# Optimization experiments

Measured on AMD Instinct MI355X. Metric: run time of the kernel, lower is better.

## Reference

```python
import jax, jax.numpy as jnp
import numpy as np

B, T, D = 2, 2048, 1024
N, H = 16, 64  # num_heads, head_dim
LOG2E = 1.442695041
NEG_INF = -1.0e9


def setup_inputs() -> dict:
    key = jax.random.key(0)
    ks = jax.random.split(key, 6)
    return {
        "input_tensor": jax.random.normal(ks[0], (B, T, D), dtype=jnp.float32),
        "attention_mask": jax.random.randint(ks[1], (B, 1, T, T), 0, 2, dtype=jnp.int32),
        "wq": jax.random.normal(ks[2], (D, N, H), dtype=jnp.float32),
        "bq": jnp.zeros((N, H), dtype=jnp.float32),
        "wk": jax.random.normal(ks[3], (D, N, H), dtype=jnp.float32),
        "bk": jnp.zeros((N, H), dtype=jnp.float32),
        "wv": jax.random.normal(ks[4], (D, N, H), dtype=jnp.float32),
        "bv": jnp.zeros((N, H), dtype=jnp.float32),
        "wo": jax.random.normal(ks[5], (D, N, H), dtype=jnp.float32),
        "bo": jnp.zeros((D,), dtype=jnp.float32),
        "per_dim_scale": jnp.zeros((H,), dtype=jnp.float32),
    }


def reference(input_tensor, attention_mask, wq, bq, wk, bk, wv, bv, wo, bo, per_dim_scale):
    # QKV projections: [B,T,D] x [D,N,H] -> [B,T,N,H]
    q = jnp.einsum('btd,dnh->btnh', input_tensor, wq) + bq
    k = jnp.einsum('btd,dnh->btnh', input_tensor, wk) + bk
    v = jnp.einsum('btd,dnh->btnh', input_tensor, wv) + bv
    # per-dim query scaling: (log2(e)/sqrt(H)) * softplus(per_dim_scale)
    scale = (LOG2E / jnp.sqrt(jnp.asarray(H, q.dtype))) * jax.nn.softplus(per_dim_scale)
    q = q * scale
    # scores: [B,N,T,S]
    scores = jnp.einsum('btnh,bsnh->bnts', q, k)
    scores = jnp.where(attention_mask == 0, jnp.asarray(NEG_INF, scores.dtype), scores)
    weights = jax.nn.softmax(scores, axis=-1)
    # AV: [B,N,T,S] x [B,S,N,H] -> [B,T,N,H]
    attn_out = jnp.einsum('bnts,bsnh->btnh', weights, v)
    # output projection: [B,T,N,H] x [D,N,H] -> [B,T,D]
    return jnp.einsum('btnh,dnh->btd', attn_out, wo) + bo
```

## Files before the change

kernel.cpp:

```cpp
#include <hip/hip_runtime.h>
#include <math.h>

typedef __bf16 bf16;
typedef __attribute__((ext_vector_type(8))) __bf16 bf16x8;
typedef __attribute__((ext_vector_type(4))) __bf16 bf16x4;
typedef __attribute__((ext_vector_type(4))) float f32x4;

#define BB 2
#define TT 2048
#define DD 1024
#define NHD 16
#define HD 64
#define MM (BB*TT)
#define LOG2E_F 1.442695041f
#define NEGINF_F (-1.0e9f)

__device__ __forceinline__ void gld16(const bf16* g, bf16* l)
{
    __builtin_amdgcn_global_load_lds(
        (const __attribute__((address_space(1))) unsigned int*)g,
        (__attribute__((address_space(3))) unsigned int*)l, 16, 0, 0);
}

__global__ __launch_bounds__(256)
void split_x(const float* __restrict__ in, bf16* __restrict__ hi,
             bf16* __restrict__ lo, int n4)
{
    int i = blockIdx.x * 256 + threadIdx.x;
    if (i < n4) {
        float4 v = ((const float4*)in)[i];
        float f[4] = {v.x, v.y, v.z, v.w};
        bf16x4 h, l;
        #pragma unroll
        for (int j = 0; j < 4; ++j) {
            bf16 hh = (bf16)f[j];
            h[j] = hh;
            l[j] = (bf16)(f[j] - (float)hh);
        }
        *(bf16x4*)(hi + (size_t)i * 4) = h;
        *(bf16x4*)(lo + (size_t)i * 4) = l;
    }
}

__global__ __launch_bounds__(256)
void prep_weights(const float* __restrict__ wq, const float* __restrict__ wk,
                  const float* __restrict__ wv, const float* __restrict__ wo,
                  bf16* __restrict__ qkh, bf16* __restrict__ qkl,
                  bf16* __restrict__ vh, bf16* __restrict__ ob)
{
    __shared__ float tile[32][33];
    const int z  = blockIdx.z;
    const int t  = threadIdx.x;
    const int r  = t >> 3;
    const int c4 = (t & 7) << 2;
    const int bx = blockIdx.x << 5;
    const int by = blockIdx.y << 5;
    if (z == 3) {
        float4 v = *(const float4*)(wo + (size_t)(by + r) * 1024 + bx + c4);
        bf16x4 o = { (bf16)v.x, (bf16)v.y, (bf16)v.z, (bf16)v.w };
        *(bf16x4*)(ob + (size_t)(by + r) * 1024 + bx + c4) = o;
        return;
    }
    const float* src = (z == 0) ? wq : ((z == 1) ? wk : wv);
    bf16* oh = (z == 0) ? qkh : ((z == 1) ? qkh + 1048576 : vh);
    bf16* ol = (z == 0) ? qkl : ((z == 1) ? qkl + 1048576 : nullptr);

    float4 v = *(const float4*)(src + (size_t)(by + r) * 1024 + bx + c4);
    tile[r][c4+0] = v.x; tile[r][c4+1] = v.y; tile[r][c4+2] = v.z; tile[r][c4+3] = v.w;
    __syncthreads();
    bf16x4 hv, lv;
    #pragma unroll
    for (int j = 0; j < 4; ++j) {
        float f = tile[c4 + j][r];
        bf16 h = (bf16)f;
        hv[j] = h;
        lv[j] = (bf16)(f - (float)h);
    }
    *(bf16x4*)(oh + (size_t)(bx + r) * 1024 + by + c4) = hv;
    if (ol)
        *(bf16x4*)(ol + (size_t)(bx + r) * 1024 + by + c4) = lv;
}

__global__ __launch_bounds__(256)
void pack_mask(const int* __restrict__ m, unsigned* __restrict__ bits, int n)
{
    int i = blockIdx.x * 256 + threadIdx.x;
    int lane = threadIdx.x & 63;
    int v = (i < n) ? m[i] : 0;
    unsigned long long b = __ballot(v != 0);
    if ((lane & 31) == 0 && i < n)
        bits[i >> 5] = (unsigned)(b >> (lane & 32));
}

__global__ __launch_bounds__(256)
void gemm128(const bf16* __restrict__ A0, const bf16* __restrict__ A1,
             const bf16* __restrict__ A2, const bf16* __restrict__ B0,
             const bf16* __restrict__ B1, const bf16* __restrict__ B2,
             const int nseg,
             const float* __restrict__ bias1, const float* __restrict__ bias2,
             const float* __restrict__ pds,
             bf16* __restrict__ oQh, bf16* __restrict__ oQl,
             bf16* __restrict__ oKh, bf16* __restrict__ oKl,
             bf16* __restrict__ oVt, float* __restrict__ oF,
             const int mode)
{
    __shared__ bf16 As[128 * 32];
    __shared__ bf16 Bs[128 * 32];

    const int t    = threadIdx.x;
    const int lane = t & 63;
    const int w    = t >> 6;
    const int quad = lane >> 4, l15 = lane & 15;
    const int m0   = blockIdx.y << 7;
    const int n0   = blockIdx.x << 7;
    const int wm   = (w >> 1) << 6;
    const int wn   = (w & 1)  << 6;

    const int jr0 = ((w * 2 + 0) << 4) + (lane >> 2);
    const int jr1 = ((w * 2 + 1) << 4) + (lane >> 2);
    const int kch = (lane & 3) << 3;

    bf16* lA0 = As + (w * 2 + 0) * 512;
    bf16* lA1 = As + (w * 2 + 1) * 512;
    bf16* lB0 = Bs + (w * 2 + 0) * 512;
    bf16* lB1 = Bs + (w * 2 + 1) * 512;

    f32x4 acc[4][4] = {};

    const bf16* Aseg[3] = {A0, A1, A2};
    const bf16* Bseg[3] = {B0, B1, B2};

    for (int seg = 0; seg < nseg; ++seg) {
        const bf16* Ap0 = Aseg[seg] + (size_t)(m0 + jr0) * DD + kch;
        const bf16* Ap1 = Aseg[seg] + (size_t)(m0 + jr1) * DD + kch;
        const bf16* Bp0 = Bseg[seg] + (size_t)(n0 + jr0) * DD + kch;
        const bf16* Bp1 = Bseg[seg] + (size_t)(n0 + jr1) * DD + kch;
        for (int k0 = 0; k0 < DD; k0 += 32) {
            __syncthreads();
            gld16(Ap0 + k0, lA0);
            gld16(Ap1 + k0, lA1);
            gld16(Bp0 + k0, lB0);
            gld16(Bp1 + k0, lB1);
            __syncthreads();
            bf16x8 af[4], bfm[4];
            #pragma unroll
            for (int mt = 0; mt < 4; ++mt)
                af[mt] = *(const bf16x8*)(As + (wm + (mt << 4) + l15) * 32 + (quad << 3));
            #pragma unroll
            for (int nt = 0; nt < 4; ++nt)
                bfm[nt] = *(const bf16x8*)(Bs + (wn + (nt << 4) + l15) * 32 + (quad << 3));
            #pragma unroll
            for (int mt = 0; mt < 4; ++mt)
                #pragma unroll
                for (int nt = 0; nt < 4; ++nt)
                    acc[mt][nt] = __builtin_amdgcn_mfma_f32_16x16x32_bf16(
                        af[mt], bfm[nt], acc[mt][nt], 0, 0, 0);
        }
    }

    if (mode == 0) {
        #pragma unroll
        for (int nt = 0; nt < 4; ++nt) {
            const int col = n0 + wn + (nt << 4) + l15;
            const int isQ = (col < 1024);
            const int nh  = col & 1023;
            const int n   = nh >> 6, h = nh & 63;
            const float bcol = isQ ? bias1[nh] : bias2[nh];
            float s = 1.f;
            if (isQ) {
                float x  = pds[h];
                float sp = fmaxf(x, 0.f) + log1pf(expf(-fabsf(x)));
                s = (LOG2E_F * LOG2E_F / 8.0f) * sp;
            }
            bf16* dH = isQ ? oQh : oKh;
            bf16* dL = isQ ? oQl : oKl;
            #pragma unroll
            for (int mt = 0; mt < 4; ++mt) {
                #pragma unroll
                for (int reg = 0; reg < 4; ++reg) {
                    const int row = m0 + wm + (mt << 4) + (quad << 2) + reg;
                    const int bi  = row >> 11;
                    const int tt  = row & (TT - 1);
                    float val = (acc[mt][nt][reg] + bcol) * s;
                    const size_t idx = (((size_t)bi * NHD + n) * TT + tt) * HD + h;
                    bf16 hi = (bf16)val;
                    dH[idx] = hi;
                    dL[idx] = (bf16)(val - (float)hi);
                }
            }
        }
    } else if (mode == 1) {
        #pragma unroll
        for (int nt = 0; nt < 4; ++nt) {
            const int col = n0 + wn + (nt << 4) + l15;
            const int bi  = col >> 11;
            const int tt  = col & (TT - 1);
            #pragma unroll
            for (int mt = 0; mt < 4; ++mt) {
                #pragma unroll
                for (int reg = 0; reg < 4; ++reg) {
                    const int row = m0 + wm + (mt << 4) + (quad << 2) + reg;
                    float val = acc[mt][nt][reg] + bias1[row];
                    oVt[((size_t)bi * 1024 + row) * TT + tt] = (bf16)val;
                }
            }
        }
    } else {
        #pragma unroll
        for (int nt = 0; nt < 4; ++nt) {
            const int col = n0 + wn + (nt << 4) + l15;
            const float bcol = bias2[col];
            #pragma unroll
            for (int mt = 0; mt < 4; ++mt) {
                #pragma unroll
                for (int reg = 0; reg < 4; ++reg) {
                    const int row = m0 + wm + (mt << 4) + (quad << 2) + reg;
                    oF[(size_t)row * DD + col] = acc[mt][nt][reg] + bcol;
                }
            }
        }
    }
}

__global__ __launch_bounds__(256)
void attn_mfma(const bf16* __restrict__ Qh, const bf16* __restrict__ Ql,
               const bf16* __restrict__ Kh, const bf16* __restrict__ Kl,
               const bf16* __restrict__ Vt, const unsigned* __restrict__ mbits,
               bf16* __restrict__ AO)
{
    __shared__ bf16 Ksh[64][72];
    __shared__ bf16 Ksl[64][72];
    __shared__ bf16 Vts[64][72];
    __shared__ bf16 Ps[4][16][72];
    __shared__ unsigned msk[64][2];

    const int t    = threadIdx.x;
    const int lane = t & 63;
    const int w    = t >> 6;
    const int quad = lane >> 4, l15 = lane & 15;
    const int bn   = blockIdx.y;
    const int b    = bn >> 4, n = bn & 15;
    const int q0   = blockIdx.x << 6;

    const bf16* Qbh = Qh + (size_t)bn * TT * HD;
    const bf16* Qbl = Ql + (size_t)bn * TT * HD;
    const bf16* Kbh = Kh + (size_t)bn * TT * HD;
    const bf16* Kbl = Kl + (size_t)bn * TT * HD;
    const bf16* Vtb = Vt + (size_t)bn * HD * TT;

    const int qrow = q0 + (w << 4) + l15;
    bf16x8 qfh[2], qfl[2];
    qfh[0] = *(const bf16x8*)(Qbh + (size_t)qrow * HD + (quad << 3));
    qfh[1] = *(const bf16x8*)(Qbh + (size_t)qrow * HD + 32 + (quad << 3));
    qfl[0] = *(const bf16x8*)(Qbl + (size_t)qrow * HD + (quad << 3));
    qfl[1] = *(const bf16x8*)(Qbl + (size_t)qrow * HD + 32 + (quad << 3));

    f32x4 O[4];
    #pragma unroll
    for (int i = 0; i < 4; ++i) O[i] = (f32x4){0.f,0.f,0.f,0.f};
    float m_i = -INFINITY;
    float l_i = 0.f;

    const int rS = t >> 2, cS = (t & 3) << 4;

    for (int kb = 0; kb < TT; kb += 64) {
        const bf16* kph = Kbh + (size_t)(kb + rS) * HD + cS;
        const bf16* kpl = Kbl + (size_t)(kb + rS) * HD + cS;
        bf16x8 kh0 = *(const bf16x8*)kph;
        bf16x8 kh1 = *(const bf16x8*)(kph + 8);
        bf16x8 kl0 = *(const bf16x8*)kpl;
        bf16x8 kl1 = *(const bf16x8*)(kpl + 8);
        const bf16* vp = Vtb + (size_t)rS * TT + kb + cS;
        bf16x8 v0v = *(const bf16x8*)vp;
        bf16x8 v1v = *(const bf16x8*)(vp + 8);
        unsigned mw = 0;
        if (t < 128)
            mw = mbits[((size_t)b * TT + q0 + (t >> 1)) * (TT / 32) + (kb >> 5) + (t & 1)];

        __syncthreads();
        *(bf16x8*)&Ksh[rS][cS]     = kh0;
        *(bf16x8*)&Ksh[rS][cS + 8] = kh1;
        *(bf16x8*)&Ksl[rS][cS]     = kl0;
        *(bf16x8*)&Ksl[rS][cS + 8] = kl1;
        *(bf16x8*)&Vts[rS][cS]     = v0v;
        *(bf16x8*)&Vts[rS][cS + 8] = v1v;
        if (t < 128) msk[t >> 1][t & 1] = mw;
        __syncthreads();

        f32x4 s_acc[4];
        #pragma unroll
        for (int i = 0; i < 4; ++i) s_acc[i] = (f32x4){0.f,0.f,0.f,0.f};
        #pragma unroll
        for (int k2 = 0; k2 < 2; ++k2) {
            #pragma unroll
            for (int nt = 0; nt < 4; ++nt) {
                bf16x8 bkh = *(const bf16x8*)&Ksh[(nt << 4) + l15][(k2 << 5) + (quad << 3)];
                bf16x8 bkl = *(const bf16x8*)&Ksl[(nt << 4) + l15][(k2 << 5) + (quad << 3)];
                s_acc[nt] = __builtin_amdgcn_mfma_f32_16x16x32_bf16(bkh, qfh[k2], s_acc[nt], 0, 0, 0);
                s_acc[nt] = __builtin_amdgcn_mfma_f32_16x16x32_bf16(bkl, qfh[k2], s_acc[nt], 0, 0, 0);
                s_acc[nt] = __builtin_amdgcn_mfma_f32_16x16x32_bf16(bkh, qfl[k2], s_acc[nt], 0, 0, 0);
            }
        }

        const unsigned w0 = msk[(w << 4) + l15][0];
        const unsigned w1 = msk[(w << 4) + l15][1];
        float sv[16];
        #pragma unroll
        for (int nt = 0; nt < 4; ++nt) {
            const unsigned word = (nt & 2) ? w1 : w0;
            #pragma unroll
            for (int reg = 0; reg < 4; ++reg) {
                const int bit = ((nt & 1) << 4) + (quad << 2) + reg;
                sv[nt * 4 + reg] = ((word >> bit) & 1u) ? s_acc[nt][reg] : NEGINF_F;
            }
        }
        float mx = sv[0];
        #pragma unroll
        for (int i = 1; i < 16; ++i) mx = fmaxf(mx, sv[i]);
        mx = fmaxf(mx, __shfl_xor(mx, 16));
        mx = fmaxf(mx, __shfl_xor(mx, 32));
        const float mnew  = fmaxf(m_i, mx);
        const float alpha = exp2f(m_i - mnew);
        float p[16], sum = 0.f;
        #pragma unroll
        for (int i = 0; i < 16; ++i) { p[i] = exp2f(sv[i] - mnew); sum += p[i]; }
        sum += __shfl_xor(sum, 16);
        sum += __shfl_xor(sum, 32);
        l_i = l_i * alpha + sum;
        m_i = mnew;
        #pragma unroll
        for (int nt = 0; nt < 4; ++nt) {
            O[nt][0] *= alpha; O[nt][1] *= alpha;
            O[nt][2] *= alpha; O[nt][3] *= alpha;
            #pragma unroll
            for (int reg = 0; reg < 4; ++reg)
                Ps[w][l15][(nt << 4) + (quad << 2) + reg] = (bf16)p[nt * 4 + reg];
        }

        #pragma unroll
        for (int s2 = 0; s2 < 2; ++s2) {
            bf16x8 ap = *(const bf16x8*)&Ps[w][l15][(s2 << 5) + (quad << 3)];
            #pragma unroll
            for (int nt = 0; nt < 4; ++nt) {
                bf16x8 bv = *(const bf16x8*)&Vts[(nt << 4) + l15][(s2 << 5) + (quad << 3)];
                O[nt] = __builtin_amdgcn_mfma_f32_16x16x32_bf16(bv, ap, O[nt], 0, 0, 0);
            }
        }
    }

    {
        const float inv = 1.0f / l_i;
        const size_t base = ((size_t)b * TT + qrow) * (NHD * HD) + (size_t)n * HD;
        #pragma unroll
        for (int nt = 0; nt < 4; ++nt) {
            bf16x4 o = { (bf16)(O[nt][0] * inv), (bf16)(O[nt][1] * inv),
                         (bf16)(O[nt][2] * inv), (bf16)(O[nt][3] * inv) };
            *(bf16x4*)(AO + base + (nt << 4) + (quad << 2)) = o;
        }
    }
}

extern "C" void kernel_launch(void* const* d_in, const int* in_sizes, int n_in,
                              void* d_out, int out_size, void* d_ws, size_t ws_size,
                              hipStream_t stream)
{
    const float* X   = (const float*)d_in[0];
    const int*   msk = (const int*)d_in[1];
    const float* wq  = (const float*)d_in[2];
    const float* bq  = (const float*)d_in[3];
    const float* wk  = (const float*)d_in[4];
    const float* bk  = (const float*)d_in[5];
    const float* wv  = (const float*)d_in[6];
    const float* bv  = (const float*)d_in[7];
    const float* wo  = (const float*)d_in[8];
    const float* bo  = (const float*)d_in[9];
    const float* pds = (const float*)d_in[10];
    float* out = (float*)d_out;

    bf16* ws   = (bf16*)d_ws;
    bf16* Xh   = ws;
    bf16* Xl   = ws + 4194304;
    bf16* WQKh = ws + 8388608;
    bf16* WQKl = ws + 10485760;
    bf16* Wvh  = ws + 12582912;
    bf16* Wob  = ws + 13631488;
    bf16* Qhb  = ws + 14680064;
    bf16* Qlb  = ws + 18874368;
    bf16* Khb  = ws + 23068672;
    bf16* Klb  = ws + 27262976;
    unsigned* mbits = (unsigned*)(ws + 31457280);
    bf16* Vtb  = Xl;
    bf16* AOb  = Xh;

    dim3 blk(256);

    split_x<<<4096, blk, 0, stream>>>(X, Xh, Xl, MM * DD / 4);
    prep_weights<<<dim3(32, 32, 4), blk, 0, stream>>>(wq, wk, wv, wo,
                                                      WQKh, WQKl, Wvh, Wob);
    pack_mask<<<32768, blk, 0, stream>>>(msk, mbits, BB * TT * TT);

    gemm128<<<dim3(16, 32), blk, 0, stream>>>(
        Xh, Xh, Xl, WQKh, WQKl, WQKh, 3, bq, bk, pds,
        Qhb, Qlb, Khb, Klb, nullptr, nullptr, 0);

    gemm128<<<dim3(32, 8), blk, 0, stream>>>(
        Wvh, nullptr, nullptr, Xh, nullptr, nullptr, 1, bv, nullptr, nullptr,
        nullptr, nullptr, nullptr, nullptr, Vtb, nullptr, 1);

    dim3 ga(TT / 64, BB * NHD);
    attn_mfma<<<ga, blk, 0, stream>>>(Qhb, Qlb, Khb, Klb, Vtb, mbits, AOb);

    gemm128<<<dim3(8, 32), blk, 0, stream>>>(
        AOb, nullptr, nullptr, Wob, nullptr, nullptr, 1, nullptr, bo, nullptr,
        nullptr, nullptr, nullptr, nullptr, nullptr, out, 2);
}
```

Before: 366.7 us.

## Merge prep kernels into one launch and fuse split-bf16 QK GEMM segments

Replaces three preprocessing kernels (X split, weight transpose/split, mask packing) with a single launch dispatched by block index, which removes launch gaps. The QK projection gets a dedicated kernel that loads hi and lo tiles of X and W together in each k-step and issues three MFMA passes per tile. Before, the three split-precision segments ran as separate k loops. This cuts the number of barriers and k-loop iterations, at the cost of twice the LDS per block, which may lower occupancy. The attention kernel also now writes P to LDS with vectorized bf16x4 stores instead of scalar stores.

Measured after the change: 344.5 us. 1.06x faster.

```diff
diff --git a/kernel.cpp b/kernel.cpp
--- a/kernel.cpp
+++ b/kernel.cpp
@@ -23,12 +23,21 @@
 }
 
 __global__ __launch_bounds__(256)
-void split_x(const float* __restrict__ in, bf16* __restrict__ hi,
-             bf16* __restrict__ lo, int n4)
-{
-    int i = blockIdx.x * 256 + threadIdx.x;
-    if (i < n4) {
-        float4 v = ((const float4*)in)[i];
+void prep_all(const float* __restrict__ X, const int* __restrict__ m,
+              const float* __restrict__ wq, const float* __restrict__ wk,
+              const float* __restrict__ wv, const float* __restrict__ wo,
+              bf16* __restrict__ Xh, bf16* __restrict__ Xl,
+              bf16* __restrict__ qkh, bf16* __restrict__ qkl,
+              bf16* __restrict__ vh, bf16* __restrict__ ob,
+              unsigned* __restrict__ bits)
+{
+    __shared__ float tile[32][33];
+    const int bid = blockIdx.x;
+    const int t   = threadIdx.x;
+
+    if (bid < 4096) {
+        int i = bid * 256 + t;
+        float4 v = ((const float4*)X)[i];
         float f[4] = {v.x, v.y, v.z, v.w};
         bf16x4 h, l;
         #pragma unroll
@@ -37,75 +46,65 @@
             h[j] = hh;
             l[j] = (bf16)(f[j] - (float)hh);
         }
-        *(bf16x4*)(hi + (size_t)i * 4) = h;
-        *(bf16x4*)(lo + (size_t)i * 4) = l;
+        *(bf16x4*)(Xh + (size_t)i * 4) = h;
+        *(bf16x4*)(Xl + (size_t)i * 4) = l;
+        return;
+    }
+    if (bid < 8192) {
+        const int idx = bid - 4096;
+        const int z   = idx >> 10;
+        const int bx  = (idx & 31) << 5;
+        const int by  = ((idx >> 5) & 31) << 5;
+        const int r   = t >> 3;
+        const int c4  = (t & 7) << 2;
+        if (z == 3) {
+            float4 v = *(const float4*)(wo + (size_t)(by + r) * 1024 + bx + c4);
+            bf16x4 o = { (bf16)v.x, (bf16)v.y, (bf16)v.z, (bf16)v.w };
+            *(bf16x4*)(ob + (size_t)(by + r) * 1024 + bx + c4) = o;
+            return;
+        }
+        const float* src = (z == 0) ? wq : ((z == 1) ? wk : wv);
+        bf16* oh = (z == 0) ? qkh : ((z == 1) ? qkh + 1048576 : vh);
+        bf16* ol = (z == 0) ? qkl : ((z == 1) ? qkl + 1048576 : nullptr);
+        float4 v = *(const float4*)(src + (size_t)(by + r) * 1024 + bx + c4);
+        tile[r][c4+0] = v.x; tile[r][c4+1] = v.y;
+        tile[r][c4+2] = v.z; tile[r][c4+3] = v.w;
+        __syncthreads();
+        bf16x4 hv, lv;
+        #pragma unroll
+        for (int j = 0; j < 4; ++j) {
+            float f = tile[c4 + j][r];
+            bf16 h = (bf16)f;
+            hv[j] = h;
+            lv[j] = (bf16)(f - (float)h);
+        }
+        *(bf16x4*)(oh + (size_t)(bx + r) * 1024 + by + c4) = hv;
+        if (ol)
+            *(bf16x4*)(ol + (size_t)(bx + r) * 1024 + by + c4) = lv;
+        return;
+    }
+    {
+        int i = (bid - 8192) * 256 + t;
+        int lane = t & 63;
+        int v = m[i];
+        unsigned long long bl = __ballot(v != 0);
+        if ((lane & 31) == 0)
+            bits[i >> 5] = (unsigned)(bl >> (lane & 32));
     }
 }
 
 __global__ __launch_bounds__(256)
-void prep_weights(const float* __restrict__ wq, const float* __restrict__ wk,
-                  const float* __restrict__ wv, const float* __restrict__ wo,
-                  bf16* __restrict__ qkh, bf16* __restrict__ qkl,
-                  bf16* __restrict__ vh, bf16* __restrict__ ob)
-{
-    __shared__ float tile[32][33];
-    const int z  = blockIdx.z;
-    const int t  = threadIdx.x;
-    const int r  = t >> 3;
-    const int c4 = (t & 7) << 2;
-    const int bx = blockIdx.x << 5;
-    const int by = blockIdx.y << 5;
-    if (z == 3) {
-        float4 v = *(const float4*)(wo + (size_t)(by + r) * 1024 + bx + c4);
-        bf16x4 o = { (bf16)v.x, (bf16)v.y, (bf16)v.z, (bf16)v.w };
-        *(bf16x4*)(ob + (size_t)(by + r) * 1024 + bx + c4) = o;
-        return;
-    }
-    const float* src = (z == 0) ? wq : ((z == 1) ? wk : wv);
-    bf16* oh = (z == 0) ? qkh : ((z == 1) ? qkh + 1048576 : vh);
-    bf16* ol = (z == 0) ? qkl : ((z == 1) ? qkl + 1048576 : nullptr);
-
-    float4 v = *(const float4*)(src + (size_t)(by + r) * 1024 + bx + c4);
-    tile[r][c4+0] = v.x; tile[r][c4+1] = v.y; tile[r][c4+2] = v.z; tile[r][c4+3] = v.w;
-    __syncthreads();
-    bf16x4 hv, lv;
-    #pragma unroll
-    for (int j = 0; j < 4; ++j) {
-        float f = tile[c4 + j][r];
-        bf16 h = (bf16)f;
-        hv[j] = h;
-        lv[j] = (bf16)(f - (float)h);
-    }
-    *(bf16x4*)(oh + (size_t)(bx + r) * 1024 + by + c4) = hv;
-    if (ol)
-        *(bf16x4*)(ol + (size_t)(bx + r) * 1024 + by + c4) = lv;
-}
-
-__global__ __launch_bounds__(256)
-void pack_mask(const int* __restrict__ m, unsigned* __restrict__ bits, int n)
-{
-    int i = blockIdx.x * 256 + threadIdx.x;
-    int lane = threadIdx.x & 63;
-    int v = (i < n) ? m[i] : 0;
-    unsigned long long b = __ballot(v != 0);
-    if ((lane & 31) == 0 && i < n)
-        bits[i >> 5] = (unsigned)(b >> (lane & 32));
-}
-
-__global__ __launch_bounds__(256)
-void gemm128(const bf16* __restrict__ A0, const bf16* __restrict__ A1,
-             const bf16* __restrict__ A2, const bf16* __restrict__ B0,
-             const bf16* __restrict__ B1, const bf16* __restrict__ B2,
-             const int nseg,
-             const float* __restrict__ bias1, const float* __restrict__ bias2,
+void gemm_qk(const bf16* __restrict__ Xh, const bf16* __restrict__ Xl,
+             const bf16* __restrict__ Wh, const bf16* __restrict__ Wl,
+             const float* __restrict__ bq, const float* __restrict__ bk,
              const float* __restrict__ pds,
              bf16* __restrict__ oQh, bf16* __restrict__ oQl,
-             bf16* __restrict__ oKh, bf16* __restrict__ oKl,
-             bf16* __restrict__ oVt, float* __restrict__ oF,
-             const int mode)
-{
-    __shared__ bf16 As[128 * 32];
-    __shared__ bf16 Bs[128 * 32];
+             bf16* __restrict__ oKh, bf16* __restrict__ oKl)
+{
+    __shared__ bf16 Ah[128 * 32];
+    __shared__ bf16 Al[128 * 32];
+    __shared__ bf16 Bh[128 * 32];
+    __shared__ bf16 Bl[128 * 32];
 
     const int t    = threadIdx.x;
     const int lane = t & 63;
@@ -120,96 +119,175 @@
     const int jr1 = ((w * 2 + 1) << 4) + (lane >> 2);
     const int kch = (lane & 3) << 3;
 
+    bf16* lAh0 = Ah + (w * 2 + 0) * 512;  bf16* lAh1 = Ah + (w * 2 + 1) * 512;
+    bf16* lAl0 = Al + (w * 2 + 0) * 512;  bf16* lAl1 = Al + (w * 2 + 1) * 512;
+    bf16* lBh0 = Bh + (w * 2 + 0) * 512;  bf16* lBh1 = Bh + (w * 2 + 1) * 512;
+    bf16* lBl0 = Bl + (w * 2 + 0) * 512;  bf16* lBl1 = Bl + (w * 2 + 1) * 512;
+
+    const bf16* pAh0 = Xh + (size_t)(m0 + jr0) * DD + kch;
+    const bf16* pAh1 = Xh + (size_t)(m0 + jr1) * DD + kch;
+    const bf16* pAl0 = Xl + (size_t)(m0 + jr0) * DD + kch;
+    const bf16* pAl1 = Xl + (size_t)(m0 + jr1) * DD + kch;
+    const bf16* pBh0 = Wh + (size_t)(n0 + jr0) * DD + kch;
+    const bf16* pBh1 = Wh + (size_t)(n0 + jr1) * DD + kch;
+    const bf16* pBl0 = Wl + (size_t)(n0 + jr0) * DD + kch;
+    const bf16* pBl1 = Wl + (size_t)(n0 + jr1) * DD + kch;
+
+    f32x4 acc[4][4] = {};
+
+    for (int k0 = 0; k0 < DD; k0 += 32) {
+        __syncthreads();
+        gld16(pAh0 + k0, lAh0);  gld16(pAh1 + k0, lAh1);
+        gld16(pAl0 + k0, lAl0);  gld16(pAl1 + k0, lAl1);
+        gld16(pBh0 + k0, lBh0);  gld16(pBh1 + k0, lBh1);
+        gld16(pBl0 + k0, lBl0);  gld16(pBl1 + k0, lBl1);
+        __syncthreads();
+
+        bf16x8 ah[4], bh[4];
+        #pragma unroll
+        for (int mt = 0; mt < 4; ++mt)
+            ah[mt] = *(const bf16x8*)(Ah + (wm + (mt << 4) + l15) * 32 + (quad << 3));
+        #pragma unroll
+        for (int nt = 0; nt < 4; ++nt)
+            bh[nt] = *(const bf16x8*)(Bh + (wn + (nt << 4) + l15) * 32 + (quad << 3));
+        #pragma unroll
+        for (int mt = 0; mt < 4; ++mt)
+            #pragma unroll
+            for (int nt = 0; nt < 4; ++nt)
+                acc[mt][nt] = __builtin_amdgcn_mfma_f32_16x16x32_bf16(
+                    ah[mt], bh[nt], acc[mt][nt], 0, 0, 0);
+
+        bf16x8 bl[4];
+        #pragma unroll
+        for (int nt = 0; nt < 4; ++nt)
+            bl[nt] = *(const bf16x8*)(Bl + (wn + (nt << 4) + l15) * 32 + (quad << 3));
+        #pragma unroll
+        for (int mt = 0; mt < 4; ++mt)
+            #pragma unroll
+            for (int nt = 0; nt < 4; ++nt)
+                acc[mt][nt] = __builtin_amdgcn_mfma_f32_16x16x32_bf16(
+                    ah[mt], bl[nt], acc[mt][nt], 0, 0, 0);
+
+        bf16x8 al[4];
+        #pragma unroll
+        for (int mt = 0; mt < 4; ++mt)
+            al[mt] = *(const bf16x8*)(Al + (wm + (mt << 4) + l15) * 32 + (quad << 3));
+        #pragma unroll
+        for (int mt = 0; mt < 4; ++mt)
+            #pragma unroll
+            for (int nt = 0; nt < 4; ++nt)
+                acc[mt][nt] = __builtin_amdgcn_mfma_f32_16x16x32_bf16(
+                    al[mt], bh[nt], acc[mt][nt], 0, 0, 0);
+    }
+
+    #pragma unroll
+    for (int nt = 0; nt < 4; ++nt) {
+        const int col = n0 + wn + (nt << 4) + l15;
+        const int isQ = (col < 1024);
+        const int nh  = col & 1023;
+        const int n   = nh >> 6, h = nh & 63;
+        const float bcol = isQ ? bq[nh] : bk[nh];
+        float s = 1.f;
+        if (isQ) {
+            float x  = pds[h];
+            float sp = fmaxf(x, 0.f) + log1pf(expf(-fabsf(x)));
+            s = (LOG2E_F * LOG2E_F / 8.0f) * sp;
+        }
+        bf16* dH = isQ ? oQh : oKh;
+        bf16* dL = isQ ? oQl : oKl;
+        #pragma unroll
+        for (int mt = 0; mt < 4; ++mt) {
+            #pragma unroll
+            for (int reg = 0; reg < 4; ++reg) {
+                const int row = m0 + wm + (mt << 4) + (quad << 2) + reg;
+                const int bi  = row >> 11;
+                const int tt  = row & (TT - 1);
+                float val = (acc[mt][nt][reg] + bcol) * s;
+                const size_t idx = (((size_t)bi * NHD + n) * TT + tt) * HD + h;
+                bf16 hi = (bf16)val;
+                dH[idx] = hi;
+                dL[idx] = (bf16)(val - (float)hi);
+            }
+        }
+    }
+}
+
+__global__ __launch_bounds__(256)
+void gemm128(const bf16* __restrict__ A, const bf16* __restrict__ Bt,
+             const float* __restrict__ bias,
+             bf16* __restrict__ oVt, float* __restrict__ oF, const int mode)
+{
+    __shared__ bf16 As[128 * 32];
+    __shared__ bf16 Bs[128 * 32];
+
+    const int t    = threadIdx.x;
+    const int lane = t & 63;
+    const int w    = t >> 6;
+    const int quad = lane >> 4, l15 = lane & 15;
+    const int m0   = blockIdx.y << 7;
+    const int n0   = blockIdx.x << 7;
+    const int wm   = (w >> 1) << 6;
+    const int wn   = (w & 1)  << 6;
+
+    const int jr0 = ((w * 2 + 0) << 4) + (lane >> 2);
+    const int jr1 = ((w * 2 + 1) << 4) + (lane >> 2);
+    const int kch = (lane & 3) << 3;
+
     bf16* lA0 = As + (w * 2 + 0) * 512;
     bf16* lA1 = As + (w * 2 + 1) * 512;
     bf16* lB0 = Bs + (w * 2 + 0) * 512;
     bf16* lB1 = Bs + (w * 2 + 1) * 512;
 
+    const bf16* Ap0 = A  + (size_t)(m0 + jr0) * DD + kch;
+    const bf16* Ap1 = A  + (size_t)(m0 + jr1) * DD + kch;
+    const bf16* Bp0 = Bt + (size_t)(n0 + jr0) * DD + kch;
+    const bf16* Bp1 = Bt + (size_t)(n0 + jr1) * DD + kch;
+
     f32x4 acc[4][4] = {};
 
-    const bf16* Aseg[3] = {A0, A1, A2};
-    const bf16* Bseg[3] = {B0, B1, B2};
-
-    for (int seg = 0; seg < nseg; ++seg) {
-        const bf16* Ap0 = Aseg[seg] + (size_t)(m0 + jr0) * DD + kch;
-        const bf16* Ap1 = Aseg[seg] + (size_t)(m0 + jr1) * DD + kch;
-        const bf16* Bp0 = Bseg[seg] + (size_t)(n0 + jr0) * DD + kch;
-        const bf16* Bp1 = Bseg[seg] + (size_t)(n0 + jr1) * DD + kch;
-        for (int k0 = 0; k0 < DD; k0 += 32) {
-            __syncthreads();
-            gld16(Ap0 + k0, lA0);
-            gld16(Ap1 + k0, lA1);
-            gld16(Bp0 + k0, lB0);
-            gld16(Bp1 + k0, lB1);
-            __syncthreads();
-            bf16x8 af[4], bfm[4];
-            #pragma unroll
-            for (int mt = 0; mt < 4; ++mt)
-                af[mt] = *(const bf16x8*)(As + (wm + (mt << 4) + l15) * 32 + (quad << 3));
+    for (int k0 = 0; k0 < DD; k0 += 32) {
+        __syncthreads();
+        gld16(Ap0 + k0, lA0);
+        gld16(Ap1 + k0, lA1);
+        gld16(Bp0 + k0, lB0);
+        gld16(Bp1 + k0, lB1);
+        __syncthreads();
+        bf16x8 af[4], bfm[4];
+        #pragma unroll
+        for (int mt = 0; mt < 4; ++mt)
+            af[mt] = *(const bf16x8*)(As + (wm + (mt << 4) + l15) * 32 + (quad << 3));
+        #pragma unroll
+        for (int nt = 0; nt < 4; ++nt)
+            bfm[nt] = *(const bf16x8*)(Bs + (wn + (nt << 4) + l15) * 32 + (quad << 3));
+        #pragma unroll
+        for (int mt = 0; mt < 4; ++mt)
             #pragma unroll
             for (int nt = 0; nt < 4; ++nt)
-                bfm[nt] = *(const bf16x8*)(Bs + (wn + (nt << 4) + l15) * 32 + (quad << 3));
-            #pragma unroll
-            for (int mt = 0; mt < 4; ++mt)
-                #pragma unroll
-                for (int nt = 0; nt < 4; ++nt)
-                    acc[mt][nt] = __builtin_amdgcn_mfma_f32_16x16x32_bf16(
-                        af[mt], bfm[nt], acc[mt][nt], 0, 0, 0);
-        }
-    }
-
-    if (mode == 0) {
+                acc[mt][nt] = __builtin_amdgcn_mfma_f32_16x16x32_bf16(
+                    af[mt], bfm[nt], acc[mt][nt], 0, 0, 0);
+    }
+
+    if (mode == 1) {
         #pragma unroll
         for (int nt = 0; nt < 4; ++nt) {
             const int col = n0 + wn + (nt << 4) + l15;
-            const int isQ = (col < 1024);
-            const int nh  = col & 1023;
-            const int n   = nh >> 6, h = nh & 63;
-            const float bcol = isQ ? bias1[nh] : bias2[nh];
-            float s = 1.f;
-            if (isQ) {
-                float x  = pds[h];
-                float sp = fmaxf(x, 0.f) + log1pf(expf(-fabsf(x)));
-                s = (LOG2E_F * LOG2E_F / 8.0f) * sp;
-            }
-            bf16* dH = isQ ? oQh : oKh;
-            bf16* dL = isQ ? oQl : oKl;
+            const int bi  = col >> 11;
+            const int tt  = col & (TT - 1);
             #pragma unroll
             for (int mt = 0; mt < 4; ++mt) {
                 #pragma unroll
                 for (int reg = 0; reg < 4; ++reg) {
                     const int row = m0 + wm + (mt << 4) + (quad << 2) + reg;
-                    const int bi  = row >> 11;
-                    const int tt  = row & (TT - 1);
-                    float val = (acc[mt][nt][reg] + bcol) * s;
-                    const size_t idx = (((size_t)bi * NHD + n) * TT + tt) * HD + h;
-                    bf16 hi = (bf16)val;
-                    dH[idx] = hi;
-                    dL[idx] = (bf16)(val - (float)hi);
+                    float val = acc[mt][nt][reg] + bias[row];
+                    oVt[((size_t)bi * 1024 + row) * TT + tt] = (bf16)val;
                 }
             }
         }
-    } else if (mode == 1) {
+    } else {
         #pragma unroll
         for (int nt = 0; nt < 4; ++nt) {
             const int col = n0 + wn + (nt << 4) + l15;
-            const int bi  = col >> 11;
-            const int tt  = col & (TT - 1);
-            #pragma unroll
-            for (int mt = 0; mt < 4; ++mt) {
-                #pragma unroll
-                for (int reg = 0; reg < 4; ++reg) {
-                    const int row = m0 + wm + (mt << 4) + (quad << 2) + reg;
-                    float val = acc[mt][nt][reg] + bias1[row];
-                    oVt[((size_t)bi * 1024 + row) * TT + tt] = (bf16)val;
-                }
-            }
-        }
-    } else {
-        #pragma unroll
-        for (int nt = 0; nt < 4; ++nt) {
-            const int col = n0 + wn + (nt << 4) + l15;
-            const float bcol = bias2[col];
+            const float bcol = bias[col];
             #pragma unroll
             for (int mt = 0; mt < 4; ++mt) {
                 #pragma unroll
@@ -332,9 +410,9 @@
         for (int nt = 0; nt < 4; ++nt) {
             O[nt][0] *= alpha; O[nt][1] *= alpha;
             O[nt][2] *= alpha; O[nt][3] *= alpha;
-            #pragma unroll
-            for (int reg = 0; reg < 4; ++reg)
-                Ps[w][l15][(nt << 4) + (quad << 2) + reg] = (bf16)p[nt * 4 + reg];
+            bf16x4 pv = { (bf16)p[nt * 4 + 0], (bf16)p[nt * 4 + 1],
+                          (bf16)p[nt * 4 + 2], (bf16)p[nt * 4 + 3] };
+            *(bf16x4*)&Ps[w][l15][(nt << 4) + (quad << 2)] = pv;
         }
 
         #pragma unroll
@@ -394,23 +472,18 @@
 
     dim3 blk(256);
 
-    split_x<<<4096, blk, 0, stream>>>(X, Xh, Xl, MM * DD / 4);
-    prep_weights<<<dim3(32, 32, 4), blk, 0, stream>>>(wq, wk, wv, wo,
-                                                      WQKh, WQKl, Wvh, Wob);
-    pack_mask<<<32768, blk, 0, stream>>>(msk, mbits, BB * TT * TT);
-
-    gemm128<<<dim3(16, 32), blk, 0, stream>>>(
-        Xh, Xh, Xl, WQKh, WQKl, WQKh, 3, bq, bk, pds,
-        Qhb, Qlb, Khb, Klb, nullptr, nullptr, 0);
+    prep_all<<<40960, blk, 0, stream>>>(X, msk, wq, wk, wv, wo,
+                                        Xh, Xl, WQKh, WQKl, Wvh, Wob, mbits);
+
+    gemm_qk<<<dim3(16, 32), blk, 0, stream>>>(
+        Xh, Xl, WQKh, WQKl, bq, bk, pds, Qhb, Qlb, Khb, Klb);
 
     gemm128<<<dim3(32, 8), blk, 0, stream>>>(
-        Wvh, nullptr, nullptr, Xh, nullptr, nullptr, 1, bv, nullptr, nullptr,
-        nullptr, nullptr, nullptr, nullptr, Vtb, nullptr, 1);
+        Wvh, Xh, bv, Vtb, nullptr, 1);
 
     dim3 ga(TT / 64, BB * NHD);
     attn_mfma<<<ga, blk, 0, stream>>>(Qhb, Qlb, Khb, Klb, Vtb, mbits, AOb);
 
     gemm128<<<dim3(8, 32), blk, 0, stream>>>(
-        AOb, nullptr, nullptr, Wob, nullptr, nullptr, 1, nullptr, bo, nullptr,
-        nullptr, nullptr, nullptr, nullptr, nullptr, out, 2);
-}
+        AOb, Wob, bo, nullptr, out, 2);
+}
```
